# Kernel optimization log

Measured on AMD Instinct MI355X. Metric: run time of the kernel, lower is better.

Reference implementation:

```python
import jax, jax.numpy as jnp
import numpy as np

BASE_WEIGHT = 0.01
ADAPTATION_RATE = 0.1
EPS = 1e-8
N = 16384
H = 64


def setup_inputs() -> dict:
    key = jax.random.key(0)
    k1, k2, k3, k4 = jax.random.split(key, 4)
    return {
        "x_input": jax.random.normal(k1, (N,), dtype=jnp.float32),
        "targets": jax.random.normal(k2, (N,), dtype=jnp.float32),
        "w1": jax.random.normal(k3, (H,), dtype=jnp.float32) * 0.5,
        "b1": jnp.zeros((H,), dtype=jnp.float32),
        "w2": jax.random.normal(k4, (H,), dtype=jnp.float32) * 0.5,
        "b2": jnp.zeros((1,), dtype=jnp.float32),
    }


def _mlp(x, w1, b1, w2, b2):
    # elementwise 1 -> H -> 1 tanh MLP: predictions y_i = f(x_i)
    h = jnp.tanh(x[:, None] * w1 + b1)  # [N, H]
    return h @ w2 + b2[0]               # [N]


def _local_density(x):
    # NxN pairwise abs-diff matrix, top-3 smallest per row
    diff = jnp.abs(x[:, None] - x[None, :]) + EPS       # [N, N]
    neg_knn, _ = jax.lax.top_k(-diff, 3)                # smallest 3 via negation
    knn = -neg_knn                                       # [N, 3]
    dens = 1.0 / (knn.mean(axis=1, keepdims=True) + EPS)  # [N, 1]
    return dens / (dens.max() + EPS)


def reference(x_input, targets, w1, b1, w2, b2):
    f_sum = lambda xx: jnp.sum(_mlp(xx, w1, b1, w2, b2))
    predictions = _mlp(x_input, w1, b1, w2, b2)
    mse_loss = jnp.mean((predictions - targets) ** 2)

    # torch.autograd.grad(..., grad_outputs=ones) twice == grad of summed output twice
    dy_dx_sum = lambda xx: jnp.sum(jax.grad(f_sum)(xx))
    d2y_dx2 = jax.grad(dy_dx_sum)(x_input)               # [N]

    density = _local_density(x_input)                    # [N, 1]
    adaptive_weights = 1.0 + ADAPTATION_RATE * density   # [N, 1]
    # torch broadcasts [N,1]*[N] -> [N,N]; mean of that outer product equals
    # mean(weights) * mean(d2**2) exactly, so compute it without the NxN alloc.
    curvature_penalty = BASE_WEIGHT * (jnp.mean(adaptive_weights) * jnp.mean(d2y_dx2 ** 2))

    total_loss = mse_loss + curvature_penalty
    return (total_loss, mse_loss, curvature_penalty)
```

## Files before the change

kernel.cpp:

```cpp
#include <hip/hip_runtime.h>
#include <math.h>

#define NPTS 16384
#define HDIM 64
#define JCH 32
#define CHUNK (NPTS / JCH)
#define IBLK 256
#define NIB (NPTS / IBLK)
#define EPSF 1e-8f
#define FMAX3 3.402823466e38f

__device__ __forceinline__ void ins2(float& m1, float& m2, float d) {
    m2 = __builtin_amdgcn_fmed3f(d, m1, m2);
    m1 = fminf(d, m1);
}

__global__ __launch_bounds__(IBLK) void knn2_kernel(
    const float* __restrict__ x, float2* __restrict__ part,
    float* __restrict__ acc) {
    const int jc = blockIdx.x & (JCH - 1);
    const int ic = blockIdx.x >> 5;
    if (blockIdx.x == 0 && threadIdx.x < 8) acc[threadIdx.x] = 0.0f;
    const int i = ic * IBLK + threadIdx.x;
    const float xi = x[i];
    const float* __restrict__ xc = x + jc * CHUNK;

    float m1 = FMAX3, m2 = FMAX3;
    if (jc == (ic >> 1)) {
        float m3 = FMAX3;
#pragma unroll 16
        for (int k = 0; k < CHUNK; ++k) {
            float d = fabsf(xi - xc[k]);
            m3 = __builtin_amdgcn_fmed3f(d, m2, m3);
            m2 = __builtin_amdgcn_fmed3f(d, m1, m2);
            m1 = fminf(d, m1);
        }
        m1 = m2;
        m2 = m3;
    } else {
#pragma unroll 16
        for (int k = 0; k < CHUNK; ++k) {
            float d = fabsf(xi - xc[k]);
            ins2(m1, m2, d);
        }
    }
    part[jc * NPTS + i] = make_float2(m1, m2);
}

__global__ __launch_bounds__(64) void merge_kernel(
    const float* __restrict__ x, const float* __restrict__ tg,
    const float* __restrict__ w1, const float* __restrict__ b1,
    const float* __restrict__ w2, const float* __restrict__ b2,
    const float2* __restrict__ part, float* __restrict__ acc,
    float* __restrict__ out) {
    const int t = threadIdx.x;
    const int i = blockIdx.x * 64 + t;

    float m1 = FMAX3, m2 = FMAX3;
#pragma unroll
    for (int jc = 0; jc < JCH; ++jc) {
        float2 p = part[jc * NPTS + i];
        ins2(m1, m2, p.x);
        ins2(m1, m2, p.y);
    }
    float dens = 1.0f / ((m1 + m2) * (1.0f / 3.0f) + 2.0f * EPSF);

    const float xi = x[i];
    float y = b2[0];
    float d2a = 0.0f;
#pragma unroll 8
    for (int j = 0; j < HDIM; ++j) {
        float a1 = w1[j], bb = b1[j], a2 = w2[j];
        float u = fmaf(xi, a1, bb);
        float e = __expf(2.0f * u);
        float r = __builtin_amdgcn_rcpf(e + 1.0f);
        float tt = fmaf(-2.0f, r, 1.0f);
        y = fmaf(a2, tt, y);
        float g = 2.0f * tt * fmaf(tt, tt, -1.0f);
        d2a = fmaf(a2 * a1 * a1, g, d2a);
    }
    float diff = y - tg[i];
    float rs_mse = diff * diff;
    float rs_d2 = d2a * d2a;
    float rs_dn = dens, rmx = dens;
    for (int o = 32; o > 0; o >>= 1) {
        rs_mse += __shfl_down(rs_mse, o);
        rs_d2 += __shfl_down(rs_d2, o);
        rs_dn += __shfl_down(rs_dn, o);
        rmx = fmaxf(rmx, __shfl_down(rmx, o));
    }
    if (t == 0) {
        atomicAdd(&acc[0], rs_mse);
        atomicAdd(&acc[1], rs_d2);
        atomicAdd(&acc[2], rs_dn);
        atomicMax((unsigned int*)&acc[3], __float_as_uint(rmx));
        __threadfence();
        unsigned int ticket = atomicAdd((unsigned int*)&acc[4], 1u);
        if (ticket == (NPTS / 64) - 1) {
            float s_mse = atomicAdd(&acc[0], 0.0f);
            float s_d2 = atomicAdd(&acc[1], 0.0f);
            float s_dn = atomicAdd(&acc[2], 0.0f);
            float dmax = __uint_as_float(atomicMax((unsigned int*)&acc[3], 0u));
            float mse = s_mse * (1.0f / NPTS);
            float md2 = s_d2 * (1.0f / NPTS);
            float mean_density = (s_dn * (1.0f / NPTS)) / (dmax + EPSF);
            float penalty = 0.01f * (1.0f + 0.1f * mean_density) * md2;
            out[0] = mse + penalty;
            out[1] = mse;
            out[2] = penalty;
        }
    }
}

extern "C" void kernel_launch(void* const* d_in, const int* in_sizes, int n_in,
                              void* d_out, int out_size, void* d_ws, size_t ws_size,
                              hipStream_t stream) {
    const float* x = (const float*)d_in[0];
    const float* tg = (const float*)d_in[1];
    const float* w1 = (const float*)d_in[2];
    const float* b1 = (const float*)d_in[3];
    const float* w2 = (const float*)d_in[4];
    const float* b2 = (const float*)d_in[5];
    float* out = (float*)d_out;
    float* wsf = (float*)d_ws;
    float2* part = (float2*)wsf;
    float* acc = wsf + 2 * JCH * NPTS;

    hipLaunchKernelGGL(knn2_kernel, dim3(NIB * JCH), dim3(IBLK), 0, stream, x, part, acc);
    hipLaunchKernelGGL(merge_kernel, dim3(NPTS / 64), dim3(64), 0, stream,
                       x, tg, w1, b1, w2, b2, part, acc, out);
}
```

Before: 104.9 us.

## Replace brute-force pairwise kNN with bucket sort and sorted-neighbor lookup

```diff
diff --git a/kernel.cpp b/kernel.cpp
--- a/kernel.cpp
+++ b/kernel.cpp
@@ -3,67 +3,118 @@
 
 #define NPTS 16384
 #define HDIM 64
-#define JCH 32
-#define CHUNK (NPTS / JCH)
-#define IBLK 256
-#define NIB (NPTS / IBLK)
+#define NBINS 32768
+#define XLO -8.0f
+#define INVW 2048.0f
 #define EPSF 1e-8f
 #define FMAX3 3.402823466e38f
+
+__device__ __forceinline__ int bin_of(float v) {
+    int b = (int)((v - XLO) * INVW);
+    return min(max(b, 0), NBINS - 1);
+}
 
 __device__ __forceinline__ void ins2(float& m1, float& m2, float d) {
     m2 = __builtin_amdgcn_fmed3f(d, m1, m2);
     m1 = fminf(d, m1);
 }
 
-__global__ __launch_bounds__(IBLK) void knn2_kernel(
-    const float* __restrict__ x, float2* __restrict__ part,
-    float* __restrict__ acc) {
-    const int jc = blockIdx.x & (JCH - 1);
-    const int ic = blockIdx.x >> 5;
-    if (blockIdx.x == 0 && threadIdx.x < 8) acc[threadIdx.x] = 0.0f;
-    const int i = ic * IBLK + threadIdx.x;
-    const float xi = x[i];
-    const float* __restrict__ xc = x + jc * CHUNK;
+__global__ __launch_bounds__(256) void hist_kernel(
+    const float* __restrict__ x, unsigned* __restrict__ hist) {
+    const int i = blockIdx.x * 256 + threadIdx.x;
+    atomicAdd(&hist[bin_of(x[i])], 1u);
+}
 
-    float m1 = FMAX3, m2 = FMAX3;
-    if (jc == (ic >> 1)) {
-        float m3 = FMAX3;
-#pragma unroll 16
-        for (int k = 0; k < CHUNK; ++k) {
-            float d = fabsf(xi - xc[k]);
-            m3 = __builtin_amdgcn_fmed3f(d, m2, m3);
-            m2 = __builtin_amdgcn_fmed3f(d, m1, m2);
-            m1 = fminf(d, m1);
+__global__ __launch_bounds__(1024) void prefix_kernel(
+    const unsigned* __restrict__ hist, unsigned* __restrict__ cursor) {
+    const int t = threadIdx.x;
+    const int base = t * 32;
+    unsigned c[32];
+#pragma unroll
+    for (int k = 0; k < 32; ++k) c[k] = hist[base + k];
+    unsigned s = 0;
+#pragma unroll
+    for (int k = 0; k < 32; ++k) { unsigned v = c[k]; c[k] = s; s += v; }
+    unsigned inc = s;
+    const int lane = t & 63;
+#pragma unroll
+    for (int o = 1; o < 64; o <<= 1) {
+        unsigned n = __shfl_up(inc, o);
+        if (lane >= o) inc += n;
+    }
+    __shared__ unsigned wsum[16];
+    const int wv = t >> 6;
+    if (lane == 63) wsum[wv] = inc;
+    __syncthreads();
+    unsigned woff = 0;
+#pragma unroll
+    for (int k = 0; k < 16; ++k) woff += (k < wv) ? wsum[k] : 0u;
+    const unsigned excl = woff + inc - s;
+#pragma unroll
+    for (int k = 0; k < 32; ++k) cursor[base + k] = excl + c[k];
+}
+
+__global__ __launch_bounds__(256) void scatter_kernel(
+    const float* __restrict__ x, unsigned* __restrict__ cursor,
+    float* __restrict__ vals) {
+    const int i = blockIdx.x * 256 + threadIdx.x;
+    const float v = x[i];
+    const unsigned pos = atomicAdd(&cursor[bin_of(v)], 1u);
+    vals[pos] = v;
+}
+
+__global__ __launch_bounds__(256) void binsort_kernel(
+    const unsigned* __restrict__ cursor, float* __restrict__ vals) {
+    const int b = blockIdx.x * 256 + threadIdx.x;
+    const unsigned s = (b > 0) ? cursor[b - 1] : 0u;
+    const unsigned e = cursor[b];
+    const unsigned n = e - s;
+    if (n < 2u) return;
+    if (n <= 16u) {
+        float r[16];
+#pragma unroll
+        for (int k = 0; k < 16; ++k)
+            r[k] = (k < (int)n) ? vals[s + k] : FMAX3;
+#pragma unroll
+        for (int rd = 0; rd < 16; ++rd) {
+#pragma unroll
+            for (int j = (rd & 1); j + 1 < 16; j += 2) {
+                float lo = fminf(r[j], r[j + 1]);
+                float hi = fmaxf(r[j], r[j + 1]);
+                r[j] = lo; r[j + 1] = hi;
+            }
         }
-        m1 = m2;
-        m2 = m3;
+#pragma unroll
+        for (int k = 0; k < 16; ++k)
+            if (k < (int)n) vals[s + k] = r[k];
     } else {
-#pragma unroll 16
-        for (int k = 0; k < CHUNK; ++k) {
-            float d = fabsf(xi - xc[k]);
-            ins2(m1, m2, d);
+        for (unsigned a = s + 1; a < e; ++a) {
+            float key = vals[a];
+            unsigned j = a;
+            while (j > s && vals[j - 1] > key) { vals[j] = vals[j - 1]; --j; }
+            vals[j] = key;
         }
     }
-    part[jc * NPTS + i] = make_float2(m1, m2);
 }
 
-__global__ __launch_bounds__(64) void merge_kernel(
+__global__ __launch_bounds__(64) void final_kernel(
     const float* __restrict__ x, const float* __restrict__ tg,
     const float* __restrict__ w1, const float* __restrict__ b1,
     const float* __restrict__ w2, const float* __restrict__ b2,
-    const float2* __restrict__ part, float* __restrict__ acc,
+    const float* __restrict__ vals, float* __restrict__ acc,
     float* __restrict__ out) {
     const int t = threadIdx.x;
     const int i = blockIdx.x * 64 + t;
 
-    float m1 = FMAX3, m2 = FMAX3;
-#pragma unroll
-    for (int jc = 0; jc < JCH; ++jc) {
-        float2 p = part[jc * NPTS + i];
-        ins2(m1, m2, p.x);
-        ins2(m1, m2, p.y);
-    }
-    float dens = 1.0f / ((m1 + m2) * (1.0f / 3.0f) + 2.0f * EPSF);
+    const float vp = vals[i];
+    const float dm1 = (i >= 1) ? vp - vals[i - 1] : FMAX3;
+    const float dm2 = (i >= 2) ? vp - vals[i - 2] : FMAX3;
+    const float dp1 = (i + 1 < NPTS) ? vals[i + 1] - vp : FMAX3;
+    const float dp2 = (i + 2 < NPTS) ? vals[i + 2] - vp : FMAX3;
+    const float m1 = fminf(dm1, dp1);
+    const float s2 = (dm1 <= dp1) ? dm2 : dp2;
+    const float m2 = fminf(fmaxf(dm1, dp1), s2);
+    const float dens = 1.0f / ((m1 + m2) * (1.0f / 3.0f) + 2.0f * EPSF);
 
     const float xi = x[i];
     float y = b2[0];
@@ -123,10 +174,17 @@
     const float* b2 = (const float*)d_in[5];
     float* out = (float*)d_out;
     float* wsf = (float*)d_ws;
-    float2* part = (float2*)wsf;
-    float* acc = wsf + 2 * JCH * NPTS;
 
-    hipLaunchKernelGGL(knn2_kernel, dim3(NIB * JCH), dim3(IBLK), 0, stream, x, part, acc);
-    hipLaunchKernelGGL(merge_kernel, dim3(NPTS / 64), dim3(64), 0, stream,
-                       x, tg, w1, b1, w2, b2, part, acc, out);
+    float* acc = wsf;
+    unsigned* hist = (unsigned*)(wsf + 8);
+    unsigned* cursor = hist + NBINS;
+    float* vals = (float*)(cursor + NBINS);
+
+    hipMemsetAsync(d_ws, 0, (8 + NBINS) * sizeof(float), stream);
+    hipLaunchKernelGGL(hist_kernel, dim3(NPTS / 256), dim3(256), 0, stream, x, hist);
+    hipLaunchKernelGGL(prefix_kernel, dim3(1), dim3(1024), 0, stream, hist, cursor);
+    hipLaunchKernelGGL(scatter_kernel, dim3(NPTS / 256), dim3(256), 0, stream, x, cursor, vals);
+    hipLaunchKernelGGL(binsort_kernel, dim3(NBINS / 256), dim3(256), 0, stream, cursor, vals);
+    hipLaunchKernelGGL(final_kernel, dim3(NPTS / 64), dim3(64), 0, stream,
+                       x, tg, w1, b1, w2, b2, vals, acc, out);
 }
```

After: 105.8 us. Within noise of the previous version (+0.8%).

## Replace brute-force pairwise kNN with uniform-grid binned neighbor search

Applied to the files above, without the earlier changes.

```diff
diff --git a/kernel.cpp b/kernel.cpp
--- a/kernel.cpp
+++ b/kernel.cpp
@@ -3,69 +3,75 @@
 
 #define NPTS 16384
 #define HDIM 64
-#define JCH 32
-#define CHUNK (NPTS / JCH)
-#define IBLK 256
-#define NIB (NPTS / IBLK)
+#define NBINS 32768
+#define CAP 32
+#define XLO -8.0f
+#define INVW 2048.0f
+#define BINW (1.0f / INVW)
 #define EPSF 1e-8f
 #define FMAX3 3.402823466e38f
+
+__device__ __forceinline__ int bin_of(float v) {
+    int b = (int)((v - XLO) * INVW);
+    return min(max(b, 0), NBINS - 1);
+}
 
 __device__ __forceinline__ void ins2(float& m1, float& m2, float d) {
     m2 = __builtin_amdgcn_fmed3f(d, m1, m2);
     m1 = fminf(d, m1);
 }
 
-__global__ __launch_bounds__(IBLK) void knn2_kernel(
-    const float* __restrict__ x, float2* __restrict__ part,
-    float* __restrict__ acc) {
-    const int jc = blockIdx.x & (JCH - 1);
-    const int ic = blockIdx.x >> 5;
-    if (blockIdx.x == 0 && threadIdx.x < 8) acc[threadIdx.x] = 0.0f;
-    const int i = ic * IBLK + threadIdx.x;
-    const float xi = x[i];
-    const float* __restrict__ xc = x + jc * CHUNK;
-
-    float m1 = FMAX3, m2 = FMAX3;
-    if (jc == (ic >> 1)) {
-        float m3 = FMAX3;
-#pragma unroll 16
-        for (int k = 0; k < CHUNK; ++k) {
-            float d = fabsf(xi - xc[k]);
-            m3 = __builtin_amdgcn_fmed3f(d, m2, m3);
-            m2 = __builtin_amdgcn_fmed3f(d, m1, m2);
-            m1 = fminf(d, m1);
-        }
-        m1 = m2;
-        m2 = m3;
-    } else {
-#pragma unroll 16
-        for (int k = 0; k < CHUNK; ++k) {
-            float d = fabsf(xi - xc[k]);
-            ins2(m1, m2, d);
-        }
-    }
-    part[jc * NPTS + i] = make_float2(m1, m2);
+__global__ __launch_bounds__(256) void scatter_kernel(
+    const float* __restrict__ x, unsigned* __restrict__ cnt,
+    float* __restrict__ slots, unsigned* __restrict__ pos) {
+    const int i = blockIdx.x * 256 + threadIdx.x;
+    const float v = x[i];
+    const int b = bin_of(v);
+    const unsigned r = atomicAdd(&cnt[b], 1u);
+    const unsigned s = ((unsigned)b << 5) + r;
+    if (r < CAP) slots[s] = v;
+    pos[i] = s;
 }
 
-__global__ __launch_bounds__(64) void merge_kernel(
+__global__ __launch_bounds__(64) void final_kernel(
     const float* __restrict__ x, const float* __restrict__ tg,
     const float* __restrict__ w1, const float* __restrict__ b1,
     const float* __restrict__ w2, const float* __restrict__ b2,
-    const float2* __restrict__ part, float* __restrict__ acc,
+    const unsigned* __restrict__ cnt, const float* __restrict__ slots,
+    const unsigned* __restrict__ pos, float* __restrict__ acc,
     float* __restrict__ out) {
     const int t = threadIdx.x;
     const int i = blockIdx.x * 64 + t;
 
+    const float v = x[i];
+    const unsigned self = pos[i];
+    const int b = (int)(self >> 5);
     float m1 = FMAX3, m2 = FMAX3;
-#pragma unroll
-    for (int jc = 0; jc < JCH; ++jc) {
-        float2 p = part[jc * NPTS + i];
-        ins2(m1, m2, p.x);
-        ins2(m1, m2, p.y);
+    {
+        const unsigned n = min(cnt[b], (unsigned)CAP);
+        const unsigned base = (unsigned)b << 5;
+        for (unsigned r = 0; r < n; ++r) {
+            const unsigned s = base + r;
+            if (s != self) ins2(m1, m2, fabsf(v - slots[s]));
+        }
     }
-    float dens = 1.0f / ((m1 + m2) * (1.0f / 3.0f) + 2.0f * EPSF);
+    int kL = b - 1, kR = b + 1;
+    for (;;) {
+        const bool hasL = (kL >= 0), hasR = (kR < NBINS);
+        if (!hasL && !hasR) break;
+        const float lbL = hasL ? (v - fmaf((float)(kL + 1), BINW, XLO)) : FMAX3;
+        const float lbR = hasR ? (fmaf((float)kR, BINW, XLO) - v) : FMAX3;
+        if (fminf(lbL, lbR) - BINW >= m2) break;
+        int bb;
+        if (lbL <= lbR) { bb = kL; --kL; } else { bb = kR; ++kR; }
+        const unsigned n = min(cnt[bb], (unsigned)CAP);
+        const unsigned base = (unsigned)bb << 5;
+        for (unsigned r = 0; r < n; ++r)
+            ins2(m1, m2, fabsf(v - slots[base + r]));
+    }
+    const float dens = 1.0f / ((m1 + m2) * (1.0f / 3.0f) + 2.0f * EPSF);
 
-    const float xi = x[i];
+    const float xi = v;
     float y = b2[0];
     float d2a = 0.0f;
 #pragma unroll 8
@@ -123,10 +129,15 @@
     const float* b2 = (const float*)d_in[5];
     float* out = (float*)d_out;
     float* wsf = (float*)d_ws;
-    float2* part = (float2*)wsf;
-    float* acc = wsf + 2 * JCH * NPTS;
 
-    hipLaunchKernelGGL(knn2_kernel, dim3(NIB * JCH), dim3(IBLK), 0, stream, x, part, acc);
-    hipLaunchKernelGGL(merge_kernel, dim3(NPTS / 64), dim3(64), 0, stream,
-                       x, tg, w1, b1, w2, b2, part, acc, out);
+    float* acc = wsf;
+    unsigned* cnt = (unsigned*)(wsf + 8);
+    unsigned* pos = cnt + NBINS;
+    float* slots = (float*)(pos + NPTS);
+
+    hipMemsetAsync(d_ws, 0, (8 + NBINS) * sizeof(float), stream);
+    hipLaunchKernelGGL(scatter_kernel, dim3(NPTS / 256), dim3(256), 0, stream,
+                       x, cnt, slots, pos);
+    hipLaunchKernelGGL(final_kernel, dim3(NPTS / 64), dim3(64), 0, stream,
+                       x, tg, w1, b1, w2, b2, cnt, slots, pos, acc, out);
 }
```

After: 249.9 us. 2.38x slower.
